# Kernel tuning notes

Measured on AMD Instinct MI355X. Metric: run time of the kernel, lower is better.

Reference implementation:

```python
import jax, jax.numpy as jnp
import numpy as np

LEVELS = 100
TIMESTAMPS = 32768
DIM = 2048
N = 32768
SIG_MIN, SIG_MAX = -3.0, 3.0


def _bipolar(key, shape):
    return jnp.where(jax.random.uniform(key, shape) < 0.5, -1.0, 1.0).astype(jnp.float32)


def setup_inputs() -> dict:
    key = jax.random.key(0)
    ks = jax.random.split(key, 11)
    # (t, x, y, z): sorted times in [0, TIMESTAMPS), gaussian signals
    times = jnp.sort(jax.random.uniform(ks[0], (N,), minval=0.0, maxval=float(TIMESTAMPS)))
    # ensure strictly increasing so jerk dt != 0
    times = times + jnp.arange(N, dtype=jnp.float32) * 1e-3
    xyz = jax.random.normal(ks[1], (N, 3), dtype=jnp.float32)
    inp = jnp.concatenate([times[:, None], xyz], axis=1)  # [N,4]
    return {
        "input": inp,
        "W_x": _bipolar(ks[2], (LEVELS, DIM)),
        "W_y": _bipolar(ks[3], (LEVELS, DIM)),
        "W_z": _bipolar(ks[4], (LEVELS, DIM)),
        "W_mag": _bipolar(ks[5], (LEVELS, DIM)),
        "W_xj": _bipolar(ks[6], (LEVELS, DIM)),
        "W_yj": _bipolar(ks[7], (LEVELS, DIM)),
        "W_zj": _bipolar(ks[8], (LEVELS, DIM)),
        "W_magj": _bipolar(ks[9], (LEVELS, DIM)),
        "W_t": _bipolar(ks[10], (TIMESTAMPS, DIM)),
    }


def _level_lookup(table, value, low, high):
    # torchhd Level: map value in [low, high] to index in [0, n-1], clamp, gather
    n = table.shape[0]
    idx = jnp.round((value - low) / (high - low) * (n - 1)).astype(jnp.int32)
    idx = jnp.clip(idx, 0, n - 1)
    return table[idx]  # [N, DIM]


def reference(input, W_x, W_y, W_z, W_mag, W_xj, W_yj, W_zj, W_magj, W_t):
    t = input[:, 0] - input[0, 0]
    x = jnp.clip(input[:, 1], SIG_MIN, SIG_MAX)
    y = jnp.clip(input[:, 2], SIG_MIN, SIG_MAX)
    z = jnp.clip(input[:, 3], SIG_MIN, SIG_MAX)
    x_lv = _level_lookup(W_x, x, SIG_MIN, SIG_MAX)
    y_lv = _level_lookup(W_y, y, SIG_MIN, SIG_MAX)
    z_lv = _level_lookup(W_z, z, SIG_MIN, SIG_MAX)
    mags = jnp.sqrt(jnp.sum(input[:, 1:] ** 2, axis=1))
    mag_lv = _level_lookup(W_mag, mags, SIG_MIN, SIG_MAX)
    # vectorized jerk: row 0 is zeros (matches the original's initial zeros row)
    dt = t[1:] - t[:-1]
    jerk = jnp.concatenate(
        [jnp.zeros((1, 3), input.dtype), (input[1:, 1:] - input[:-1, 1:]) / dt[:, None]],
        axis=0,
    )  # [N,3]
    xj = jnp.clip(jerk[:, 0], SIG_MIN, SIG_MAX)
    yj = jnp.clip(jerk[:, 1], SIG_MIN, SIG_MAX)
    zj = jnp.clip(jerk[:, 2], SIG_MIN, SIG_MAX)
    xj_lv = _level_lookup(W_xj, xj, SIG_MIN, SIG_MAX)
    yj_lv = _level_lookup(W_yj, yj, SIG_MIN, SIG_MAX)
    zj_lv = _level_lookup(W_zj, zj, SIG_MIN, SIG_MAX)
    jmag = jnp.sqrt(jnp.sum(jerk ** 2, axis=1))
    jmag_lv = _level_lookup(W_magj, jmag, SIG_MIN, SIG_MAX)
    t_lv = _level_lookup(W_t, t, 0.0, float(TIMESTAMPS))
    sample_hvs = ((x_lv + y_lv + z_lv) * mag_lv + (xj_lv + yj_lv + zj_lv) * jmag_lv) * t_lv
    return jnp.tanh(jnp.sum(sample_hvs, axis=0))  # [DIM] multiset + tanh
```

## Files before the change

### kernel.cpp

```cpp
#include <hip/hip_runtime.h>
#include <hip/hip_bf16.h>
#include <math.h>

#define DIM     2048
#define LEVELS  100
#define TSN     32768
#define NSPLIT  32
#define NBLK    1024
#define PACK_BLOCKS 200

__device__ __forceinline__ int lvl100(float v) {
    float f = ((v + 3.0f) / 6.0f) * 99.0f;
    int k = (int)rintf(f);
    return min(max(k, 0), LEVELS - 1);
}

__global__ __launch_bounds__(256) void prep_k(
    const float* __restrict__ w0, const float* __restrict__ w1,
    const float* __restrict__ w2, const float* __restrict__ w3,
    const float* __restrict__ w4, const float* __restrict__ w5,
    const float* __restrict__ w6, const float* __restrict__ w7,
    const float* __restrict__ inp,
    unsigned int* __restrict__ packed2,
    unsigned long long* __restrict__ sidx,
    unsigned int* __restrict__ tidx, int n)
{
    if (blockIdx.x < PACK_BLOCKS) {
        int tab = blockIdx.x / 25;
        int lg  = blockIdx.x - tab * 25;
        int l   = threadIdx.x & 63;
        int level = lg * 4 + (threadIdx.x >> 6);
        const float* w;
        switch (tab) {
            case 0: w = w0; break; case 1: w = w1; break;
            case 2: w = w2; break; case 3: w = w3; break;
            case 4: w = w4; break; case 5: w = w5; break;
            case 6: w = w6; break; default: w = w7; break;
        }
        const float* base = w + (size_t)level * DIM + 4 * l;
        unsigned int word = 0;
        #pragma unroll
        for (int k = 0; k < 8; ++k) {
            float4 a = *(const float4*)(base + 256 * k);
            word |= (a.x < 0.f ? 1u : 0u) << (4 * k);
            word |= (a.y < 0.f ? 1u : 0u) << (4 * k + 1);
            word |= (a.z < 0.f ? 1u : 0u) << (4 * k + 2);
            word |= (a.w < 0.f ? 1u : 0u) << (4 * k + 3);
        }
        packed2[(tab * LEVELS + level) * 64 + l] = word;
        return;
    }
    int i = (blockIdx.x - PACK_BLOCKS) * 256 + threadIdx.x;
    if (i >= n) return;
    float t0 = inp[0];
    float ti = inp[i * 4] - t0;
    float x = inp[i * 4 + 1], y = inp[i * 4 + 2], z = inp[i * 4 + 3];
    float xc = fminf(fmaxf(x, -3.f), 3.f);
    float yc = fminf(fmaxf(y, -3.f), 3.f);
    float zc = fminf(fmaxf(z, -3.f), 3.f);
    unsigned long long ix = (unsigned long long)lvl100(xc);
    unsigned long long iy = (unsigned long long)lvl100(yc);
    unsigned long long iz = (unsigned long long)lvl100(zc);
    float mag = sqrtf((x * x + y * y) + z * z);
    unsigned long long im = (unsigned long long)lvl100(mag);
    float jx = 0.f, jy = 0.f, jz = 0.f;
    if (i > 0) {
        float tp = inp[(i - 1) * 4] - t0;
        float dt = ti - tp;
        jx = (x - inp[(i - 1) * 4 + 1]) / dt;
        jy = (y - inp[(i - 1) * 4 + 2]) / dt;
        jz = (z - inp[(i - 1) * 4 + 3]) / dt;
    }
    unsigned long long ixj = (unsigned long long)lvl100(fminf(fmaxf(jx, -3.f), 3.f));
    unsigned long long iyj = (unsigned long long)lvl100(fminf(fmaxf(jy, -3.f), 3.f));
    unsigned long long izj = (unsigned long long)lvl100(fminf(fmaxf(jz, -3.f), 3.f));
    float jm = sqrtf((jx * jx + jy * jy) + jz * jz);
    unsigned long long imj = (unsigned long long)lvl100(jm);
    sidx[i] = ix | (iy << 8) | (iz << 16) | (im << 24) |
              (ixj << 32) | (iyj << 40) | (izj << 48) | (imj << 56);
    float ft = (ti / 32768.0f) * 32767.0f;
    int k = (int)rintf(ft);
    tidx[i] = (unsigned int)min(max(k, 0), TSN - 1);
}

__global__ __launch_bounds__(256) void main_k(
    const float* __restrict__ Wt,
    const unsigned int* __restrict__ packed2,
    const unsigned long long* __restrict__ sidx,
    const unsigned int* __restrict__ tidx,
    float* __restrict__ partials, int spw, int n)
{
    __shared__ float red[4][DIM];
    const int tid = threadIdx.x;
    const int l   = tid & 63;
    const int wv  = tid >> 6;
    int gw = blockIdx.x * 4 + wv;
    int s0 = gw * spw;
    int s1 = min(s0 + spw, n);

    float4 acc[8];
    #pragma unroll
    for (int k = 0; k < 8; ++k) acc[k] = make_float4(0.f, 0.f, 0.f, 0.f);

    for (int s = s0; s < s1; ++s) {
        int su = __builtin_amdgcn_readfirstlane(s);
        unsigned long long sp = sidx[su];
        unsigned int ti = tidx[su];
        const float4* rowp = (const float4*)(Wt + (size_t)ti * DIM);

        unsigned int i_x  = (unsigned int)(sp)       & 0xffu;
        unsigned int i_y  = (unsigned int)(sp >> 8)  & 0xffu;
        unsigned int i_z  = (unsigned int)(sp >> 16) & 0xffu;
        unsigned int i_m  = (unsigned int)(sp >> 24) & 0xffu;
        unsigned int i_xj = (unsigned int)(sp >> 32) & 0xffu;
        unsigned int i_yj = (unsigned int)(sp >> 40) & 0xffu;
        unsigned int i_zj = (unsigned int)(sp >> 48) & 0xffu;
        unsigned int i_mj = (unsigned int)(sp >> 56) & 0xffu;

        unsigned int Bx  = packed2[(0 * LEVELS + i_x ) * 64 + l];
        unsigned int By  = packed2[(1 * LEVELS + i_y ) * 64 + l];
        unsigned int Bz  = packed2[(2 * LEVELS + i_z ) * 64 + l];
        unsigned int Bm  = packed2[(3 * LEVELS + i_m ) * 64 + l];
        unsigned int Bxj = packed2[(4 * LEVELS + i_xj) * 64 + l];
        unsigned int Byj = packed2[(5 * LEVELS + i_yj) * 64 + l];
        unsigned int Bzj = packed2[(6 * LEVELS + i_zj) * 64 + l];
        unsigned int Bmj = packed2[(7 * LEVELS + i_mj) * 64 + l];

        unsigned int e1 = Bx ^ Bm,  e2 = By ^ Bm,  e3 = Bz ^ Bm;
        unsigned int e4 = Bxj ^ Bmj, e5 = Byj ^ Bmj, e6 = Bzj ^ Bmj;
        unsigned int ta  = e1 ^ e2;
        unsigned int sA  = ta ^ e3;
        unsigned int cA  = (e1 & e2) | (e3 & ta);
        unsigned int tb2 = e4 ^ e5;
        unsigned int sB  = tb2 ^ e6;
        unsigned int cB  = (e4 & e5) | (e6 & tb2);
        unsigned int ones  = sA ^ sB;
        unsigned int cc    = sA & sB;
        unsigned int tc    = cA ^ cB;
        unsigned int twos  = tc ^ cc;
        unsigned int fours = (cA & cB) | (cc & tc);

        #pragma unroll
        for (int k = 0; k < 8; ++k) {
            float4 wt4 = rowp[64 * k + l];
            #pragma unroll
            for (int j = 0; j < 4; ++j) {
                int p = 4 * k + j;
                int v = ((ones >> p) & 1) + 2 * ((twos >> p) & 1)
                      + 4 * ((fours >> p) & 1);
                float sgn = (float)(6 - 2 * v);
                float* a = (float*)&acc[k];
                float* wf = (float*)&wt4;
                a[j] = fmaf(sgn, wf[j], a[j]);
            }
        }
    }

    float4* redw = (float4*)red[wv];
    #pragma unroll
    for (int k = 0; k < 8; ++k) redw[64 * k + l] = acc[k];
    __syncthreads();

    float4 o0 = make_float4(0.f, 0.f, 0.f, 0.f);
    float4 o1 = make_float4(0.f, 0.f, 0.f, 0.f);
    #pragma unroll
    for (int r = 0; r < 4; ++r) {
        float4 a = ((float4*)red[r])[2 * tid];
        float4 b = ((float4*)red[r])[2 * tid + 1];
        o0.x += a.x; o0.y += a.y; o0.z += a.z; o0.w += a.w;
        o1.x += b.x; o1.y += b.y; o1.z += b.z; o1.w += b.w;
    }
    float4* pout = (float4*)(partials + (size_t)blockIdx.x * DIM + tid * 8);
    pout[0] = o0;
    pout[1] = o1;
}

__global__ __launch_bounds__(256) void reduce1_k(
    const float* __restrict__ partials, float* __restrict__ partial2,
    int rows_per, int nblk)
{
    int d = blockIdx.x * 256 + threadIdx.x;
    int r0 = blockIdx.y * rows_per;
    int r1 = min(r0 + rows_per, nblk);
    float s = 0.f;
    for (int b = r0; b < r1; ++b) s += partials[(size_t)b * DIM + d];
    partial2[(size_t)blockIdx.y * DIM + d] = s;
}

__global__ __launch_bounds__(256) void reduce2_k(
    const float* __restrict__ partial2, float* __restrict__ out)
{
    int d = blockIdx.x * 256 + threadIdx.x;
    float s = 0.f;
    #pragma unroll
    for (int b = 0; b < NSPLIT; ++b) s += partial2[(size_t)b * DIM + d];
    out[d] = tanhf(s);
}

extern "C" void kernel_launch(void* const* d_in, const int* in_sizes, int n_in,
                              void* d_out, int out_size, void* d_ws, size_t ws_size,
                              hipStream_t stream)
{
    const float* inp = (const float*)d_in[0];
    const float* wx  = (const float*)d_in[1];
    const float* wy  = (const float*)d_in[2];
    const float* wz  = (const float*)d_in[3];
    const float* wm  = (const float*)d_in[4];
    const float* wxj = (const float*)d_in[5];
    const float* wyj = (const float*)d_in[6];
    const float* wzj = (const float*)d_in[7];
    const float* wmj = (const float*)d_in[8];
    const float* wt  = (const float*)d_in[9];
    int n = in_sizes[0] / 4;

    char* ws = (char*)d_ws;
    unsigned int* packed2 = (unsigned int*)ws;
    size_t off = 256 * 1024;
    unsigned long long* sidx = (unsigned long long*)(ws + off);
    off += (size_t)n * 8;
    unsigned int* tidx = (unsigned int*)(ws + off);
    off += (size_t)n * 4;
    off = (off + 255) & ~(size_t)255;

    float* partial2 = (float*)(ws + off);
    off += (size_t)NSPLIT * DIM * 4;

    int nblk = NBLK;
    while (nblk > 32 && off + (size_t)nblk * DIM * 4 > ws_size) nblk >>= 1;
    float* partials = (float*)(ws + off);

    int idx_blocks = (n + 255) / 256;
    hipLaunchKernelGGL(prep_k, dim3(PACK_BLOCKS + idx_blocks), dim3(256), 0, stream,
                       wx, wy, wz, wm, wxj, wyj, wzj, wmj,
                       inp, packed2, sidx, tidx, n);
    int spw = (n + nblk * 4 - 1) / (nblk * 4);
    hipLaunchKernelGGL(main_k, dim3(nblk), dim3(256), 0, stream,
                       wt, packed2, sidx, tidx, partials, spw, n);
    int rows_per = (nblk + NSPLIT - 1) / NSPLIT;
    hipLaunchKernelGGL(reduce1_k, dim3(DIM / 256, NSPLIT), dim3(256), 0, stream,
                       partials, partial2, rows_per, nblk);
    hipLaunchKernelGGL(reduce2_k, dim3(DIM / 256), dim3(256), 0, stream,
                       partial2, (float*)d_out);
}
```

Measured before the change: 55.10 us.

## Reuse W_t rows across repeated timestamps, prefetch indices, fuse reductions with atomic counter

The main kernel now prefetches the next sample's packed indices and keeps the current W_t row in registers, reloading it only when the timestamp index changes. Because the times are sorted and many samples round to the same index, this cuts repeated global row loads. The two reduction kernels are merged into one: the last block per column, found through an atomic counter, computes the final sum and tanh. This needs an extra memset launch and threadfence synchronisation, and holding the row in registers raises register pressure.

```diff
diff --git a/kernel.cpp b/kernel.cpp
--- a/kernel.cpp
+++ b/kernel.cpp
@@ -5,8 +5,8 @@
 #define DIM     2048
 #define LEVELS  100
 #define TSN     32768
+#define NBLK    1024
 #define NSPLIT  32
-#define NBLK    1024
 #define PACK_BLOCKS 200
 
 __device__ __forceinline__ int lvl100(float v) {
@@ -101,21 +101,37 @@
     float4 acc[8];
     #pragma unroll
     for (int k = 0; k < 8; ++k) acc[k] = make_float4(0.f, 0.f, 0.f, 0.f);
+    float4 row[8];
+    unsigned int ti_prev = 0xffffffffu;
+
+    unsigned long long sp = 0ull; unsigned int ti = 0u;
+    if (s0 < s1) {
+        int su = __builtin_amdgcn_readfirstlane(s0);
+        sp = sidx[su]; ti = tidx[su];
+    }
 
     for (int s = s0; s < s1; ++s) {
-        int su = __builtin_amdgcn_readfirstlane(s);
-        unsigned long long sp = sidx[su];
-        unsigned int ti = tidx[su];
-        const float4* rowp = (const float4*)(Wt + (size_t)ti * DIM);
-
-        unsigned int i_x  = (unsigned int)(sp)       & 0xffu;
-        unsigned int i_y  = (unsigned int)(sp >> 8)  & 0xffu;
-        unsigned int i_z  = (unsigned int)(sp >> 16) & 0xffu;
-        unsigned int i_m  = (unsigned int)(sp >> 24) & 0xffu;
-        unsigned int i_xj = (unsigned int)(sp >> 32) & 0xffu;
-        unsigned int i_yj = (unsigned int)(sp >> 40) & 0xffu;
-        unsigned int i_zj = (unsigned int)(sp >> 48) & 0xffu;
-        unsigned int i_mj = (unsigned int)(sp >> 56) & 0xffu;
+        unsigned long long sp_c = sp;
+        unsigned int ti_c = ti;
+        if (s + 1 < s1) {
+            int su = __builtin_amdgcn_readfirstlane(s + 1);
+            sp = sidx[su]; ti = tidx[su];
+        }
+        if (ti_c != ti_prev) {
+            const float4* rowp = (const float4*)(Wt + (size_t)ti_c * DIM);
+            #pragma unroll
+            for (int k = 0; k < 8; ++k) row[k] = rowp[64 * k + l];
+            ti_prev = ti_c;
+        }
+
+        unsigned int i_x  = (unsigned int)(sp_c)       & 0xffu;
+        unsigned int i_y  = (unsigned int)(sp_c >> 8)  & 0xffu;
+        unsigned int i_z  = (unsigned int)(sp_c >> 16) & 0xffu;
+        unsigned int i_m  = (unsigned int)(sp_c >> 24) & 0xffu;
+        unsigned int i_xj = (unsigned int)(sp_c >> 32) & 0xffu;
+        unsigned int i_yj = (unsigned int)(sp_c >> 40) & 0xffu;
+        unsigned int i_zj = (unsigned int)(sp_c >> 48) & 0xffu;
+        unsigned int i_mj = (unsigned int)(sp_c >> 56) & 0xffu;
 
         unsigned int Bx  = packed2[(0 * LEVELS + i_x ) * 64 + l];
         unsigned int By  = packed2[(1 * LEVELS + i_y ) * 64 + l];
@@ -142,7 +158,6 @@
 
         #pragma unroll
         for (int k = 0; k < 8; ++k) {
-            float4 wt4 = rowp[64 * k + l];
             #pragma unroll
             for (int j = 0; j < 4; ++j) {
                 int p = 4 * k + j;
@@ -150,7 +165,7 @@
                       + 4 * ((fours >> p) & 1);
                 float sgn = (float)(6 - 2 * v);
                 float* a = (float*)&acc[k];
-                float* wf = (float*)&wt4;
+                float* wf = (float*)&row[k];
                 a[j] = fmaf(sgn, wf[j], a[j]);
             }
         }
@@ -175,26 +190,30 @@
     pout[1] = o1;
 }
 
-__global__ __launch_bounds__(256) void reduce1_k(
+__global__ __launch_bounds__(256) void reduce_k(
     const float* __restrict__ partials, float* __restrict__ partial2,
+    unsigned int* __restrict__ cnt, float* __restrict__ out,
     int rows_per, int nblk)
 {
-    int d = blockIdx.x * 256 + threadIdx.x;
-    int r0 = blockIdx.y * rows_per;
+    int x = blockIdx.x, y = blockIdx.y;
+    int d = x * 256 + threadIdx.x;
+    int r0 = y * rows_per;
     int r1 = min(r0 + rows_per, nblk);
     float s = 0.f;
     for (int b = r0; b < r1; ++b) s += partials[(size_t)b * DIM + d];
-    partial2[(size_t)blockIdx.y * DIM + d] = s;
-}
-
-__global__ __launch_bounds__(256) void reduce2_k(
-    const float* __restrict__ partial2, float* __restrict__ out)
-{
-    int d = blockIdx.x * 256 + threadIdx.x;
-    float s = 0.f;
-    #pragma unroll
-    for (int b = 0; b < NSPLIT; ++b) s += partial2[(size_t)b * DIM + d];
-    out[d] = tanhf(s);
+    partial2[(size_t)y * DIM + d] = s;
+    __threadfence();
+    __syncthreads();
+    __shared__ unsigned int so;
+    if (threadIdx.x == 0) so = atomicAdd(&cnt[x], 1u);
+    __syncthreads();
+    if (so == gridDim.y - 1) {
+        __threadfence();
+        float t = 0.f;
+        for (int r = 0; r < (int)gridDim.y; ++r)
+            t += partial2[(size_t)r * DIM + d];
+        out[d] = tanhf(t);
+    }
 }
 
 extern "C" void kernel_launch(void* const* d_in, const int* in_sizes, int n_in,
@@ -224,10 +243,14 @@
 
     float* partial2 = (float*)(ws + off);
     off += (size_t)NSPLIT * DIM * 4;
+    unsigned int* cnt = (unsigned int*)(ws + off);
+    off += 256;
 
     int nblk = NBLK;
     while (nblk > 32 && off + (size_t)nblk * DIM * 4 > ws_size) nblk >>= 1;
     float* partials = (float*)(ws + off);
+
+    hipMemsetAsync(cnt, 0, 8 * sizeof(unsigned int), stream);
 
     int idx_blocks = (n + 255) / 256;
     hipLaunchKernelGGL(prep_k, dim3(PACK_BLOCKS + idx_blocks), dim3(256), 0, stream,
@@ -237,8 +260,6 @@
     hipLaunchKernelGGL(main_k, dim3(nblk), dim3(256), 0, stream,
                        wt, packed2, sidx, tidx, partials, spw, n);
     int rows_per = (nblk + NSPLIT - 1) / NSPLIT;
-    hipLaunchKernelGGL(reduce1_k, dim3(DIM / 256, NSPLIT), dim3(256), 0, stream,
-                       partials, partial2, rows_per, nblk);
-    hipLaunchKernelGGL(reduce2_k, dim3(DIM / 256), dim3(256), 0, stream,
-                       partial2, (float*)d_out);
-}
+    hipLaunchKernelGGL(reduce_k, dim3(DIM / 256, NSPLIT), dim3(256), 0, stream,
+                       partials, partial2, cnt, (float*)d_out, rows_per, nblk);
+}
```

Result: slower. 79.51 us (+44.3%).
